# Kernel tuning notes

Measured on AMD Instinct MI355X. Metric: run time of the kernel, lower is better.

Reference implementation:

```python
import jax, jax.numpy as jnp
import numpy as np

B, L, D = 8, 2048, 512


def setup_inputs() -> dict:
    key = jax.random.key(0)
    ks = jax.random.split(key, 6)
    s = 0.02
    return {
        "q": jax.random.normal(ks[0], (B, L, D), jnp.float32),
        "k": jax.random.normal(ks[1], (B, L, D), jnp.float32),
        "v": jax.random.normal(ks[2], (B, L, D), jnp.float32),
        "Wq": jax.random.normal(ks[3], (D, D), jnp.float32) * s,
        "bq": jnp.zeros((D,), jnp.float32),
        "Wk": jax.random.normal(ks[4], (D, D), jnp.float32) * s,
        "bk": jnp.zeros((D,), jnp.float32),
        "Wv": jax.random.normal(ks[5], (D, D), jnp.float32) * s,
        "bv": jnp.zeros((D,), jnp.float32),
    }


def reference(q, k, v, Wq, bq, Wk, bk, Wv, bv):
    # Linear projections (torch Linear: x @ W.T + b)
    qp = jnp.einsum("bld,ed->ble", q, Wq) + bq
    kp = jnp.einsum("bld,ed->ble", k, Wk) + bk
    vp = jnp.einsum("bld,ed->ble", v, Wv) + bv
    # attn[b, i, j] = qp[b, i] . kp[b, j]   (no 1/sqrt(d) scaling in source)
    attn = jnp.einsum("bqd,bkd->bqk", qp, kp)
    # Faithful to torch.nn.Softmax(dim=1): normalize over the QUERY axis.
    attn = jax.nn.softmax(attn, axis=1)
    out = jnp.einsum("bqk,bkd->bqd", attn, vp)
    return out
```

## Files before the change

### kernel.cpp

```cpp
#include <hip/hip_runtime.h>
#include <math.h>


#define TM 128
#define TN 128
#define TKK 32

typedef __attribute__((ext_vector_type(8))) short bf16x8;
typedef __attribute__((ext_vector_type(4))) float floatx4;

typedef __attribute__((address_space(3))) short lds_short;
typedef const __attribute__((address_space(1))) short glob_short;

__device__ __forceinline__ short f2bf(float x) {
    unsigned u = __float_as_uint(x);
    u += 0x7fff + ((u >> 16) & 1);
    return (short)(u >> 16);
}
__device__ __forceinline__ float bf2f(short s) {
    return __uint_as_float(((unsigned)(unsigned short)s) << 16);
}

__global__ __launch_bounds__(256) void cast_f32_bf16(
    const float* __restrict__ in, short* __restrict__ out, long long n)
{
    long long i = ((long long)blockIdx.x * 256 + threadIdx.x) * 8;
    if (i + 8 > n) return;
    float4 a = *(const float4*)(in + i);
    float4 b = *(const float4*)(in + i + 4);
    bf16x8 r;
    r[0] = f2bf(a.x); r[1] = f2bf(a.y); r[2] = f2bf(a.z); r[3] = f2bf(a.w);
    r[4] = f2bf(b.x); r[5] = f2bf(b.y); r[6] = f2bf(b.z); r[7] = f2bf(b.w);
    *(bf16x8*)(out + i) = r;
}

__global__ __launch_bounds__(256) void zero_f32(float* __restrict__ p, int n)
{
    int i = blockIdx.x * 256 + threadIdx.x;
    if (i < n) p[i] = 0.f;
}

template<int HAS_BIAS, int OUT_BF16>
__global__ __launch_bounds__(256) void gemm_nt_mfma(
    const short* __restrict__ A, const short* __restrict__ B,
    const float* __restrict__ bias, void* __restrict__ C,
    int M, int N, int K,
    long long sA, long long sB, long long sC)
{
    __shared__ short As[TM * TKK];
    __shared__ short Bs[TN * TKK];
    const int bz = blockIdx.z;
    A += (long long)bz * sA;
    B += (long long)bz * sB;

    const int n0 = blockIdx.x * TN;
    const int m0 = blockIdx.y * TM;
    const int t    = threadIdx.x;
    const int wave = t >> 6;
    const int lane = t & 63;
    const int wm = (wave >> 1) * 64;
    const int wn = (wave & 1)  * 64;
    const int sr = lane >> 2;
    const int sc = (lane & 3) * 8;

    floatx4 acc[4][4];
    #pragma unroll
    for (int i = 0; i < 4; ++i)
        #pragma unroll
        for (int j = 0; j < 4; ++j)
            acc[i][j] = (floatx4){0.f, 0.f, 0.f, 0.f};

    for (int k0 = 0; k0 < K; k0 += TKK) {
        #pragma unroll
        for (int it = 0; it < 2; ++it) {
            const int chunk = it * 4 + wave;
            const int r = chunk * 16 + sr;
            __builtin_amdgcn_global_load_lds(
                (glob_short*)(A + (long long)(m0 + r) * K + k0 + sc),
                (lds_short*)(As + chunk * 512), 16, 0, 0);
            __builtin_amdgcn_global_load_lds(
                (glob_short*)(B + (long long)(n0 + r) * K + k0 + sc),
                (lds_short*)(Bs + chunk * 512), 16, 0, 0);
        }
        __syncthreads();
        bf16x8 af[4], bfr[4];
        #pragma unroll
        for (int i = 0; i < 4; ++i)
            af[i] = *(const bf16x8*)&As[(wm + i * 16 + (lane & 15)) * TKK + (lane >> 4) * 8];
        #pragma unroll
        for (int j = 0; j < 4; ++j)
            bfr[j] = *(const bf16x8*)&Bs[(wn + j * 16 + (lane & 15)) * TKK + (lane >> 4) * 8];
        #pragma unroll
        for (int i = 0; i < 4; ++i)
            #pragma unroll
            for (int j = 0; j < 4; ++j)
                acc[i][j] = __builtin_amdgcn_mfma_f32_16x16x32_bf16(af[i], bfr[j], acc[i][j], 0, 0, 0);
        __syncthreads();
    }

    #pragma unroll
    for (int i = 0; i < 4; ++i) {
        const int rbase = m0 + wm + i * 16 + (lane >> 4) * 4;
        #pragma unroll
        for (int j = 0; j < 4; ++j) {
            const int col = n0 + wn + j * 16 + (lane & 15);
            const float bb = HAS_BIAS ? bias[col] : 0.f;
            #pragma unroll
            for (int r = 0; r < 4; ++r) {
                const long long off = (long long)bz * sC + (long long)(rbase + r) * N + col;
                const float vvv = acc[i][j][r] + bb;
                if (OUT_BF16) ((short*)C)[off] = f2bf(vvv);
                else          ((float*)C)[off] = vvv;
            }
        }
    }
}

__global__ __launch_bounds__(256) void gemm_nt_exp_colsum(
    const short* __restrict__ A, const short* __restrict__ B,
    short* __restrict__ E, float* __restrict__ colsum,
    int N, int K, long long sA, long long sB, long long sE)
{
    __shared__ short As[TM * TKK];
    __shared__ short Bs[TN * TKK];
    __shared__ float wsum[4][64];
    const int bz = blockIdx.z;
    A += (long long)bz * sA;
    B += (long long)bz * sB;
    E += (long long)bz * sE;
    colsum += (long long)bz * N;

    const int n0 = blockIdx.x * TN;
    const int m0 = blockIdx.y * TM;
    const int t    = threadIdx.x;
    const int wave = t >> 6;
    const int lane = t & 63;
    const int wm = (wave >> 1) * 64;
    const int wn = (wave & 1)  * 64;
    const int sr = lane >> 2;
    const int sc = (lane & 3) * 8;

    floatx4 acc[4][4];
    #pragma unroll
    for (int i = 0; i < 4; ++i)
        #pragma unroll
        for (int j = 0; j < 4; ++j)
            acc[i][j] = (floatx4){0.f, 0.f, 0.f, 0.f};

    for (int k0 = 0; k0 < K; k0 += TKK) {
        #pragma unroll
        for (int it = 0; it < 2; ++it) {
            const int chunk = it * 4 + wave;
            const int r = chunk * 16 + sr;
            __builtin_amdgcn_global_load_lds(
                (glob_short*)(A + (long long)(m0 + r) * K + k0 + sc),
                (lds_short*)(As + chunk * 512), 16, 0, 0);
            __builtin_amdgcn_global_load_lds(
                (glob_short*)(B + (long long)(n0 + r) * K + k0 + sc),
                (lds_short*)(Bs + chunk * 512), 16, 0, 0);
        }
        __syncthreads();
        bf16x8 af[4], bfr[4];
        #pragma unroll
        for (int i = 0; i < 4; ++i)
            af[i] = *(const bf16x8*)&As[(wm + i * 16 + (lane & 15)) * TKK + (lane >> 4) * 8];
        #pragma unroll
        for (int j = 0; j < 4; ++j)
            bfr[j] = *(const bf16x8*)&Bs[(wn + j * 16 + (lane & 15)) * TKK + (lane >> 4) * 8];
        #pragma unroll
        for (int i = 0; i < 4; ++i)
            #pragma unroll
            for (int j = 0; j < 4; ++j)
                acc[i][j] = __builtin_amdgcn_mfma_f32_16x16x32_bf16(af[i], bfr[j], acc[i][j], 0, 0, 0);
        __syncthreads();
    }

    float csum[4] = {0.f, 0.f, 0.f, 0.f};
    #pragma unroll
    for (int i = 0; i < 4; ++i) {
        const int rbase = wm + i * 16 + (lane >> 4) * 4;
        #pragma unroll
        for (int j = 0; j < 4; ++j) {
            const int col = wn + j * 16 + (lane & 15);
            #pragma unroll
            for (int r = 0; r < 4; ++r) {
                const float e = __expf(acc[i][j][r]);
                E[(long long)(m0 + rbase + r) * N + (n0 + col)] = f2bf(e);
                csum[j] += e;
            }
        }
    }
    #pragma unroll
    for (int j = 0; j < 4; ++j) {
        csum[j] += __shfl_xor(csum[j], 16);
        csum[j] += __shfl_xor(csum[j], 32);
    }
    if (lane < 16) {
        #pragma unroll
        for (int j = 0; j < 4; ++j)
            wsum[wave][j * 16 + lane] = csum[j];
    }
    __syncthreads();
    if (t < 128) {
        const float s = (t < 64) ? (wsum[0][t] + wsum[2][t])
                                 : (wsum[1][t - 64] + wsum[3][t - 64]);
        atomicAdd(&colsum[n0 + t], s);
    }
}

__global__ __launch_bounds__(256) void transpose_scale_bf16(
    const short* __restrict__ in, const float* __restrict__ colsum,
    short* __restrict__ out, int R, int Cc)
{
    __shared__ short tile[32][33];
    const int b = blockIdx.z;
    in  += (long long)b * R * Cc;
    out += (long long)b * R * Cc;
    colsum += (long long)b * R;
    const int c0 = blockIdx.x * 32, r0 = blockIdx.y * 32;
    const int tx = threadIdx.x & 31, ty = threadIdx.x >> 5;
    #pragma unroll
    for (int rr = ty; rr < 32; rr += 8) {
        const float rs = 1.f / colsum[r0 + rr];
        tile[rr][tx] = f2bf(bf2f(in[(long long)(r0 + rr) * Cc + c0 + tx]) * rs);
    }
    __syncthreads();
    #pragma unroll
    for (int rr = ty; rr < 32; rr += 8)
        out[(long long)(c0 + rr) * R + r0 + tx] = tile[tx][rr];
}

extern "C" void kernel_launch(void* const* d_in, const int* in_sizes, int n_in,
                              void* d_out, int out_size, void* d_ws, size_t ws_size,
                              hipStream_t stream) {
    const float* q  = (const float*)d_in[0];
    const float* k  = (const float*)d_in[1];
    const float* v  = (const float*)d_in[2];
    const float* Wq = (const float*)d_in[3];
    const float* bq = (const float*)d_in[4];
    const float* Wk = (const float*)d_in[5];
    const float* bk = (const float*)d_in[6];
    const float* Wv = (const float*)d_in[7];
    const float* bv = (const float*)d_in[8];
    float* out = (float*)d_out;

    const int Bb = 8, L = 2048, D = 512;
    const long long BLD = (long long)Bb * L * D;
    const long long BLL = (long long)Bb * L * L;
    const long long DD  = (long long)D * D;

    short* base  = (short*)d_ws;
    short* q_bf  = base;
    short* k_bf  = q_bf  + BLD;
    short* v_bf  = k_bf  + BLD;
    short* qp_bf = v_bf  + BLD;
    short* kp_bf = qp_bf + BLD;
    short* vp_bf = kp_bf + BLD;
    short* vpT   = vp_bf + BLD;
    short* Wq_bf = vpT   + BLD;
    short* Wk_bf = Wq_bf + DD;
    short* Wv_bf = Wk_bf + DD;
    short* E_bf  = Wv_bf + DD;
    float* colsum = (float*)(E_bf + BLL);

    dim3 blk(256);

    cast_f32_bf16<<<dim3(BLD / 2048), blk, 0, stream>>>(q, q_bf, BLD);
    cast_f32_bf16<<<dim3(BLD / 2048), blk, 0, stream>>>(k, k_bf, BLD);
    cast_f32_bf16<<<dim3(BLD / 2048), blk, 0, stream>>>(v, v_bf, BLD);
    cast_f32_bf16<<<dim3(DD / 2048),  blk, 0, stream>>>(Wq, Wq_bf, DD);
    cast_f32_bf16<<<dim3(DD / 2048),  blk, 0, stream>>>(Wk, Wk_bf, DD);
    cast_f32_bf16<<<dim3(DD / 2048),  blk, 0, stream>>>(Wv, Wv_bf, DD);
    zero_f32<<<dim3((Bb * L) / 256), blk, 0, stream>>>(colsum, Bb * L);

    dim3 gproj(D / TN, (Bb * L) / TM, 1);
    gemm_nt_mfma<1, 1><<<gproj, blk, 0, stream>>>(q_bf, Wq_bf, bq, qp_bf,
                                                  Bb * L, D, D, 0, 0, 0);
    gemm_nt_mfma<1, 1><<<gproj, blk, 0, stream>>>(k_bf, Wk_bf, bk, kp_bf,
                                                  Bb * L, D, D, 0, 0, 0);
    gemm_nt_mfma<1, 1><<<gproj, blk, 0, stream>>>(v_bf, Wv_bf, bv, vp_bf,
                                                  Bb * L, D, D, 0, 0, 0);

    dim3 gS(L / TN, L / TM, Bb);
    gemm_nt_exp_colsum<<<gS, blk, 0, stream>>>(qp_bf, kp_bf, E_bf, colsum,
                                               L, D,
                                               (long long)L * D, (long long)L * D,
                                               (long long)L * L);

    dim3 gT(D / 32, L / 32, Bb);
    transpose_scale_bf16<<<gT, blk, 0, stream>>>(vp_bf, colsum, vpT, L, D);

    dim3 gO(D / TN, L / TM, Bb);
    gemm_nt_mfma<0, 0><<<gO, blk, 0, stream>>>(E_bf, vpT, nullptr, out,
                                               L, D, L,
                                               (long long)L * L, (long long)D * L,
                                               (long long)L * D);
}
```

Before: 345.6 us.

## Batch casts and QKV projections into single launches and retile PV GEMM

Merges the six cast kernels into two launches and the three projection GEMMs into one launch indexed by blockIdx.z, via a templated GEMM body. The PV GEMM uses 64x128 tiles with a 1x4 wave layout, doubling the block count to improve occupancy across CUs. Grid axes are reordered so adjacent blocks share operand rows. This reduces launch overhead and tail underutilization, at the cost of lower per-block reuse in the PV GEMM.

```diff
diff --git a/kernel.cpp b/kernel.cpp
--- a/kernel.cpp
+++ b/kernel.cpp
@@ -2,8 +2,6 @@
 #include <math.h>
 
 
-#define TM 128
-#define TN 128
 #define TKK 32
 
 typedef __attribute__((ext_vector_type(8))) short bf16x8;
@@ -21,16 +19,22 @@
     return __uint_as_float(((unsigned)(unsigned short)s) << 16);
 }
 
-__global__ __launch_bounds__(256) void cast_f32_bf16(
-    const float* __restrict__ in, short* __restrict__ out, long long n)
-{
+__global__ __launch_bounds__(256) void cast3_f32_bf16(
+    const float* __restrict__ a, const float* __restrict__ b,
+    const float* __restrict__ c,
+    short* __restrict__ oa, short* __restrict__ ob, short* __restrict__ oc,
+    long long n)
+{
+    const int z = blockIdx.y;
+    const float* in  = (z == 0) ? a  : (z == 1) ? b  : c;
+    short*       out = (z == 0) ? oa : (z == 1) ? ob : oc;
     long long i = ((long long)blockIdx.x * 256 + threadIdx.x) * 8;
     if (i + 8 > n) return;
-    float4 a = *(const float4*)(in + i);
-    float4 b = *(const float4*)(in + i + 4);
+    float4 x = *(const float4*)(in + i);
+    float4 y = *(const float4*)(in + i + 4);
     bf16x8 r;
-    r[0] = f2bf(a.x); r[1] = f2bf(a.y); r[2] = f2bf(a.z); r[3] = f2bf(a.w);
-    r[4] = f2bf(b.x); r[5] = f2bf(b.y); r[6] = f2bf(b.z); r[7] = f2bf(b.w);
+    r[0] = f2bf(x.x); r[1] = f2bf(x.y); r[2] = f2bf(x.z); r[3] = f2bf(x.w);
+    r[4] = f2bf(y.x); r[5] = f2bf(y.y); r[6] = f2bf(y.z); r[7] = f2bf(y.w);
     *(bf16x8*)(out + i) = r;
 }
 
@@ -40,74 +44,68 @@
     if (i < n) p[i] = 0.f;
 }
 
-template<int HAS_BIAS, int OUT_BF16>
-__global__ __launch_bounds__(256) void gemm_nt_mfma(
+template<int TMp, int TNp, int WM, int WN, int HAS_BIAS, int OUT_BF16>
+__device__ __forceinline__ void gemm_body(
     const short* __restrict__ A, const short* __restrict__ B,
     const float* __restrict__ bias, void* __restrict__ C,
-    int M, int N, int K,
-    long long sA, long long sB, long long sC)
-{
-    __shared__ short As[TM * TKK];
-    __shared__ short Bs[TN * TKK];
-    const int bz = blockIdx.z;
-    A += (long long)bz * sA;
-    B += (long long)bz * sB;
-
-    const int n0 = blockIdx.x * TN;
-    const int m0 = blockIdx.y * TM;
+    int N, int K, int m0, int n0)
+{
+    __shared__ short As[TMp * TKK];
+    __shared__ short Bs[TNp * TKK];
+    constexpr int MI = TMp / (16 * WM);
+    constexpr int NJ = TNp / (16 * WN);
     const int t    = threadIdx.x;
     const int wave = t >> 6;
     const int lane = t & 63;
-    const int wm = (wave >> 1) * 64;
-    const int wn = (wave & 1)  * 64;
+    const int wm = (wave / WN) * (TMp / WM);
+    const int wn = (wave % WN) * (TNp / WN);
     const int sr = lane >> 2;
     const int sc = (lane & 3) * 8;
 
-    floatx4 acc[4][4];
-    #pragma unroll
-    for (int i = 0; i < 4; ++i)
-        #pragma unroll
-        for (int j = 0; j < 4; ++j)
+    floatx4 acc[MI][NJ];
+    #pragma unroll
+    for (int i = 0; i < MI; ++i)
+        #pragma unroll
+        for (int j = 0; j < NJ; ++j)
             acc[i][j] = (floatx4){0.f, 0.f, 0.f, 0.f};
 
     for (int k0 = 0; k0 < K; k0 += TKK) {
         #pragma unroll
-        for (int it = 0; it < 2; ++it) {
-            const int chunk = it * 4 + wave;
-            const int r = chunk * 16 + sr;
+        for (int c = wave; c < TMp / 16; c += 4)
             __builtin_amdgcn_global_load_lds(
-                (glob_short*)(A + (long long)(m0 + r) * K + k0 + sc),
-                (lds_short*)(As + chunk * 512), 16, 0, 0);
+                (glob_short*)(A + (long long)(m0 + c * 16 + sr) * K + k0 + sc),
+                (lds_short*)(As + c * 512), 16, 0, 0);
+        #pragma unroll
+        for (int c = wave; c < TNp / 16; c += 4)
             __builtin_amdgcn_global_load_lds(
-                (glob_short*)(B + (long long)(n0 + r) * K + k0 + sc),
-                (lds_short*)(Bs + chunk * 512), 16, 0, 0);
-        }
+                (glob_short*)(B + (long long)(n0 + c * 16 + sr) * K + k0 + sc),
+                (lds_short*)(Bs + c * 512), 16, 0, 0);
         __syncthreads();
-        bf16x8 af[4], bfr[4];
-        #pragma unroll
-        for (int i = 0; i < 4; ++i)
+        bf16x8 af[MI], bfr[NJ];
+        #pragma unroll
+        for (int i = 0; i < MI; ++i)
             af[i] = *(const bf16x8*)&As[(wm + i * 16 + (lane & 15)) * TKK + (lane >> 4) * 8];
         #pragma unroll
-        for (int j = 0; j < 4; ++j)
+        for (int j = 0; j < NJ; ++j)
             bfr[j] = *(const bf16x8*)&Bs[(wn + j * 16 + (lane & 15)) * TKK + (lane >> 4) * 8];
         #pragma unroll
-        for (int i = 0; i < 4; ++i)
+        for (int i = 0; i < MI; ++i)
             #pragma unroll
-            for (int j = 0; j < 4; ++j)
+            for (int j = 0; j < NJ; ++j)
                 acc[i][j] = __builtin_amdgcn_mfma_f32_16x16x32_bf16(af[i], bfr[j], acc[i][j], 0, 0, 0);
         __syncthreads();
     }
 
     #pragma unroll
-    for (int i = 0; i < 4; ++i) {
+    for (int i = 0; i < MI; ++i) {
         const int rbase = m0 + wm + i * 16 + (lane >> 4) * 4;
         #pragma unroll
-        for (int j = 0; j < 4; ++j) {
+        for (int j = 0; j < NJ; ++j) {
             const int col = n0 + wn + j * 16 + (lane & 15);
             const float bb = HAS_BIAS ? bias[col] : 0.f;
             #pragma unroll
             for (int r = 0; r < 4; ++r) {
-                const long long off = (long long)bz * sC + (long long)(rbase + r) * N + col;
+                const long long off = (long long)(rbase + r) * N + col;
                 const float vvv = acc[i][j][r] + bb;
                 if (OUT_BF16) ((short*)C)[off] = f2bf(vvv);
                 else          ((float*)C)[off] = vvv;
@@ -116,13 +114,40 @@
     }
 }
 
+__global__ __launch_bounds__(256) void proj_gemm(
+    const short* __restrict__ x0, const short* __restrict__ x1, const short* __restrict__ x2,
+    const short* __restrict__ w0, const short* __restrict__ w1, const short* __restrict__ w2,
+    const float* __restrict__ b0, const float* __restrict__ b1, const float* __restrict__ b2,
+    short* __restrict__ y0, short* __restrict__ y1, short* __restrict__ y2,
+    int N, int K)
+{
+    const int z = blockIdx.z;
+    const short* A    = (z == 0) ? x0 : (z == 1) ? x1 : x2;
+    const short* B    = (z == 0) ? w0 : (z == 1) ? w1 : w2;
+    const float* bias = (z == 0) ? b0 : (z == 1) ? b1 : b2;
+    short*       C    = (z == 0) ? y0 : (z == 1) ? y1 : y2;
+    gemm_body<128, 128, 2, 2, 1, 1>(A, B, bias, C, N, K,
+                                    blockIdx.x * 128, blockIdx.y * 128);
+}
+
+__global__ __launch_bounds__(256) void pv_gemm(
+    const short* __restrict__ E, const short* __restrict__ vpT,
+    float* __restrict__ out, int N, int K,
+    long long sA, long long sB, long long sC)
+{
+    const int bz = blockIdx.z;
+    gemm_body<64, 128, 1, 4, 0, 0>(E + (long long)bz * sA, vpT + (long long)bz * sB,
+                                   nullptr, out + (long long)bz * sC, N, K,
+                                   blockIdx.x * 64, blockIdx.y * 128);
+}
+
 __global__ __launch_bounds__(256) void gemm_nt_exp_colsum(
     const short* __restrict__ A, const short* __restrict__ B,
     short* __restrict__ E, float* __restrict__ colsum,
     int N, int K, long long sA, long long sB, long long sE)
 {
-    __shared__ short As[TM * TKK];
-    __shared__ short Bs[TN * TKK];
+    __shared__ short As[128 * TKK];
+    __shared__ short Bs[128 * TKK];
     __shared__ float wsum[4][64];
     const int bz = blockIdx.z;
     A += (long long)bz * sA;
@@ -130,8 +155,8 @@
     E += (long long)bz * sE;
     colsum += (long long)bz * N;
 
-    const int n0 = blockIdx.x * TN;
-    const int m0 = blockIdx.y * TM;
+    const int m0 = blockIdx.x * 128;
+    const int n0 = blockIdx.y * 128;
     const int t    = threadIdx.x;
     const int wave = t >> 6;
     const int lane = t & 63;
@@ -265,23 +290,19 @@
 
     dim3 blk(256);
 
-    cast_f32_bf16<<<dim3(BLD / 2048), blk, 0, stream>>>(q, q_bf, BLD);
-    cast_f32_bf16<<<dim3(BLD / 2048), blk, 0, stream>>>(k, k_bf, BLD);
-    cast_f32_bf16<<<dim3(BLD / 2048), blk, 0, stream>>>(v, v_bf, BLD);
-    cast_f32_bf16<<<dim3(DD / 2048),  blk, 0, stream>>>(Wq, Wq_bf, DD);
-    cast_f32_bf16<<<dim3(DD / 2048),  blk, 0, stream>>>(Wk, Wk_bf, DD);
-    cast_f32_bf16<<<dim3(DD / 2048),  blk, 0, stream>>>(Wv, Wv_bf, DD);
+    cast3_f32_bf16<<<dim3(BLD / 2048, 3), blk, 0, stream>>>(
+        q, k, v, q_bf, k_bf, v_bf, BLD);
+    cast3_f32_bf16<<<dim3(DD / 2048, 3), blk, 0, stream>>>(
+        Wq, Wk, Wv, Wq_bf, Wk_bf, Wv_bf, DD);
     zero_f32<<<dim3((Bb * L) / 256), blk, 0, stream>>>(colsum, Bb * L);
 
-    dim3 gproj(D / TN, (Bb * L) / TM, 1);
-    gemm_nt_mfma<1, 1><<<gproj, blk, 0, stream>>>(q_bf, Wq_bf, bq, qp_bf,
-                                                  Bb * L, D, D, 0, 0, 0);
-    gemm_nt_mfma<1, 1><<<gproj, blk, 0, stream>>>(k_bf, Wk_bf, bk, kp_bf,
-                                                  Bb * L, D, D, 0, 0, 0);
-    gemm_nt_mfma<1, 1><<<gproj, blk, 0, stream>>>(v_bf, Wv_bf, bv, vp_bf,
-                                                  Bb * L, D, D, 0, 0, 0);
-
-    dim3 gS(L / TN, L / TM, Bb);
+    dim3 gproj((Bb * L) / 128, D / 128, 3);
+    proj_gemm<<<gproj, blk, 0, stream>>>(q_bf, k_bf, v_bf,
+                                         Wq_bf, Wk_bf, Wv_bf,
+                                         bq, bk, bv,
+                                         qp_bf, kp_bf, vp_bf, D, D);
+
+    dim3 gS(L / 128, L / 128, Bb);
     gemm_nt_exp_colsum<<<gS, blk, 0, stream>>>(qp_bf, kp_bf, E_bf, colsum,
                                                L, D,
                                                (long long)L * D, (long long)L * D,
@@ -290,9 +311,8 @@
     dim3 gT(D / 32, L / 32, Bb);
     transpose_scale_bf16<<<gT, blk, 0, stream>>>(vp_bf, colsum, vpT, L, D);
 
-    dim3 gO(D / TN, L / TM, Bb);
-    gemm_nt_mfma<0, 0><<<gO, blk, 0, stream>>>(E_bf, vpT, nullptr, out,
-                                               L, D, L,
-                                               (long long)L * L, (long long)D * L,
-                                               (long long)L * D);
-}
+    dim3 gO(L / 64, D / 128, Bb);
+    pv_gemm<<<gO, blk, 0, stream>>>(E_bf, vpT, out, D, L,
+                                    (long long)L * L, (long long)D * L,
+                                    (long long)L * D);
+}
```

Result: faster. 322.1 us (-6.8%).
